# Performance work log

Measured on AMD Instinct MI355X. Metric: run time of the kernel, lower is better.

Reference implementation:

```python
import jax, jax.numpy as jnp
import numpy as np

T, HID, H, KV, D = 2048, 2048, 16, 8, 128
EPS = 1e-6
THETA = 10000.0


def setup_inputs() -> dict:
    key = jax.random.key(0)
    ks = jax.random.split(key, 6)
    positions = jnp.arange(T, dtype=jnp.int64 if jax.config.jax_enable_x64 else jnp.int32)
    hidden_states = jax.random.normal(ks[0], (T, HID), dtype=jnp.float32)
    scale = 0.02
    Wq = jax.random.normal(ks[1], (HID, H * 2 * D), dtype=jnp.float32) * scale
    Wk = jax.random.normal(ks[2], (HID, KV * D), dtype=jnp.float32) * scale
    Wv = jax.random.normal(ks[3], (HID, KV * D), dtype=jnp.float32) * scale
    Wo = jax.random.normal(ks[4], (H * D, HID), dtype=jnp.float32) * scale
    q_norm_w = jnp.zeros((D,), dtype=jnp.float32)  # torch init: zeros, applied as (1+w)
    k_norm_w = jnp.zeros((D,), dtype=jnp.float32)
    return {"positions": positions, "hidden_states": hidden_states, "Wq": Wq,
            "Wk": Wk, "Wv": Wv, "Wo": Wo, "q_norm_w": q_norm_w, "k_norm_w": k_norm_w}


def _rms_norm(x, w):
    # fp32 RMSNorm with (1 + weight) scaling, per last dim
    xf = x.astype(jnp.float32)
    inv = jax.lax.rsqrt(jnp.mean(xf * xf, axis=-1, keepdims=True) + EPS)
    return (xf * inv * (1.0 + w.astype(jnp.float32))).astype(x.dtype)


def _rope(x, positions):
    # neox-style rotary over full head_dim; x: (T, heads, D)
    half = D // 2
    inv_freq = 1.0 / (THETA ** (jnp.arange(0, half, dtype=jnp.float32) / half))
    freqs = positions.astype(jnp.float32)[:, None] * inv_freq  # (T, half)
    cos = jnp.cos(freqs)[:, None, :]  # (T,1,half)
    sin = jnp.sin(freqs)[:, None, :]
    x1, x2 = x[..., :half], x[..., half:]
    return jnp.concatenate([x1 * cos - x2 * sin, x2 * cos + x1 * sin], axis=-1)


def reference(positions, hidden_states, Wq, Wk, Wv, Wo, q_norm_w, k_norm_w):
    scaling = D ** -0.5
    qg = (hidden_states @ Wq).reshape(T, H, 2 * D)
    q, gate = qg[..., :D], qg[..., D:]              # (T,H,D) each
    k = (hidden_states @ Wk).reshape(T, KV, D)
    v = (hidden_states @ Wv).reshape(T, KV, D)
    q = _rms_norm(q, q_norm_w)
    k = _rms_norm(k, k_norm_w)
    q = _rope(q, positions)
    k = _rope(k, positions)
    # GQA: repeat kv heads
    rep = H // KV
    k = jnp.repeat(k, rep, axis=1)                   # (T,H,D)
    v = jnp.repeat(v, rep, axis=1)
    scores = jnp.einsum('thd,shd->hts', q, k) * scaling  # (H,T,T)
    causal = positions[:, None] >= positions[None, :]     # (T,T)
    scores = jnp.where(causal[None], scores, jnp.finfo(scores.dtype).min)
    probs = jax.nn.softmax(scores, axis=-1)
    o = jnp.einsum('hts,shd->thd', probs, v).reshape(T, H * D)
    o = o * jax.nn.sigmoid(gate.reshape(T, H * D))
    return o @ Wo
```

## Files before the change

kernel.cpp:

```cpp
#include <hip/hip_runtime.h>
#include <stdint.h>
#include <math.h>

#define T_SEQ 2048
#define HID   2048
#define NH    16
#define NKV   8
#define DH    128

typedef __bf16 bf16x8 __attribute__((ext_vector_type(8)));
typedef float  f32x4  __attribute__((ext_vector_type(4)));

__device__ __forceinline__ ushort f2bf(float f) {
  uint32_t u = __float_as_uint(f);
  u += 0x7FFF + ((u >> 16) & 1);
  return (ushort)(u >> 16);
}
__device__ __forceinline__ ushort f2bf_rz(float f) {
  return (ushort)(__float_as_uint(f) >> 16);
}
__device__ __forceinline__ float bf2f(ushort u) {
  return __uint_as_float(((uint32_t)u) << 16);
}
__device__ __forceinline__ void gld16(const void* g, void* l) {
  __builtin_amdgcn_global_load_lds(
      (const __attribute__((address_space(1))) uint32_t*)g,
      (__attribute__((address_space(3))) uint32_t*)l, 16, 0, 0);
}

__global__ __launch_bounds__(256) void prep_kernel(
    const float* __restrict__ hs, const float* __restrict__ Wq,
    const float* __restrict__ Wk, const float* __restrict__ Wv,
    const float* __restrict__ Wo, ushort* __restrict__ hs16,
    ushort* __restrict__ Wqt, ushort* __restrict__ Wkt,
    ushort* __restrict__ Wvt, ushort* __restrict__ Wot) {
  int bid = blockIdx.x;
  if (bid < 4096) {
    int i = (bid * 256 + threadIdx.x) * 4;
    float4 v = *(const float4*)(hs + i);
    ushort4 o = {f2bf(v.x), f2bf(v.y), f2bf(v.z), f2bf(v.w)};
    *(ushort4*)(hs16 + i) = o;
    return;
  }
  bid -= 4096;
  const float* src; ushort* dst; int N, bi, bj;
  if (bid < 2048)      { src = Wq; dst = Wqt; N = 4096; bj = bid & 63; bi = bid >> 6; }
  else if (bid < 2560) { bid -= 2048; src = Wk; dst = Wkt; N = 1024; bj = bid & 15; bi = bid >> 4; }
  else if (bid < 3072) { bid -= 2560; src = Wv; dst = Wvt; N = 1024; bj = bid & 15; bi = bid >> 4; }
  else                 { bid -= 3072; src = Wo; dst = Wot; N = 2048; bj = bid & 31; bi = bid >> 5; }
  __shared__ float tile[64][65];
  const int r = threadIdx.x >> 2, cg = (threadIdx.x & 3) * 16;
  const float* sp = src + (size_t)(bi * 64 + r) * N + bj * 64 + cg;
#pragma unroll
  for (int p = 0; p < 4; ++p) {
    float4 v = *(const float4*)(sp + p * 4);
    tile[r][cg + p * 4 + 0] = v.x; tile[r][cg + p * 4 + 1] = v.y;
    tile[r][cg + p * 4 + 2] = v.z; tile[r][cg + p * 4 + 3] = v.w;
  }
  __syncthreads();
  ushort* dp = dst + (size_t)(bj * 64 + r) * HID + bi * 64 + cg;
#pragma unroll
  for (int p = 0; p < 2; ++p) {
    union { uint4 v; ushort u[8]; } o;
#pragma unroll
    for (int j = 0; j < 8; ++j) o.u[j] = f2bf(tile[cg + p * 8 + j][r]);
    *(uint4*)(dp + p * 8) = o.v;
  }
}

template <int MI>
__device__ __forceinline__ void gemm_loop(
    const ushort* __restrict__ A, const ushort* __restrict__ Bt,
    int K, int m0, int n0, ushort* As, ushort* Bs, f32x4 (*acc)[4]) {
  const int tid = threadIdx.x, lane = tid & 63, w = tid >> 6;
  const int quad = lane >> 4, l15 = lane & 15;
  const int wm = (w >> 1) * (MI * 16), wn = (w & 1) * 64;
  const int srow = tid >> 2, sch = tid & 3;
  for (int k0 = 0; k0 < K; k0 += 32) {
    __syncthreads();
#pragma unroll
    for (int p = 0; p < MI / 2; ++p) {
      int row = p * 64 + srow;
      int gch = sch ^ ((row >> 1) & 3);
      gld16(A + (size_t)(m0 + row) * K + k0 + gch * 8,
            As + (p * 256 + w * 64) * 8);
    }
#pragma unroll
    for (int p = 0; p < 2; ++p) {
      int row = p * 64 + srow;
      int gch = sch ^ ((row >> 1) & 3);
      gld16(Bt + (size_t)(n0 + row) * K + k0 + gch * 8,
            Bs + (p * 256 + w * 64) * 8);
    }
    __syncthreads();
    bf16x8 af[MI], bfr[4];
#pragma unroll
    for (int mi = 0; mi < MI; ++mi) {
      int row = wm + mi * 16 + l15;
      int pch = quad ^ ((row >> 1) & 3);
      af[mi] = *(const bf16x8*)(As + row * 32 + pch * 8);
    }
#pragma unroll
    for (int ni = 0; ni < 4; ++ni) {
      int row = wn + ni * 16 + l15;
      int pch = quad ^ ((row >> 1) & 3);
      bfr[ni] = *(const bf16x8*)(Bs + row * 32 + pch * 8);
    }
#pragma unroll
    for (int mi = 0; mi < MI; ++mi)
#pragma unroll
      for (int ni = 0; ni < 4; ++ni)
        acc[mi][ni] = __builtin_amdgcn_mfma_f32_16x16x32_bf16(
            af[mi], bfr[ni], acc[mi][ni], 0, 0, 0);
  }
}

__device__ __forceinline__ void bf16_store(f32x4 (*acc)[4],
                                           ushort* __restrict__ Cb, int Ncols,
                                           int m0, int n0) {
  const int lane = threadIdx.x & 63, w = threadIdx.x >> 6;
  const int quad = lane >> 4, l15 = lane & 15;
  const int wm = (w >> 1) * 64, wn = (w & 1) * 64;
#pragma unroll
  for (int mi = 0; mi < 4; ++mi)
#pragma unroll
    for (int ni = 0; ni < 4; ++ni)
#pragma unroll
      for (int r = 0; r < 4; ++r) {
        int row = m0 + wm + mi * 16 + quad * 4 + r;
        int col = n0 + wn + ni * 16 + l15;
        Cb[(size_t)row * Ncols + col] = f2bf(acc[mi][ni][r]);
      }
}

__global__ __launch_bounds__(256) void gemm_qkv(
    const ushort* __restrict__ hs16, const ushort* __restrict__ Wqt,
    const ushort* __restrict__ Wkt, const ushort* __restrict__ Wvt,
    ushort* __restrict__ q16, ushort* __restrict__ gate16,
    ushort* __restrict__ k16, ushort* __restrict__ v16t) {
  __shared__ ushort As[128 * 32];
  __shared__ ushort Bs[128 * 32];
  f32x4 acc[4][4];
#pragma unroll
  for (int i = 0; i < 4; ++i)
#pragma unroll
    for (int j = 0; j < 4; ++j) acc[i][j] = (f32x4){0.f, 0.f, 0.f, 0.f};
  const int b = blockIdx.x;
  if (b < 512) {
    int mt = b >> 5, nt = b & 31, m0 = mt * 128;
    gemm_loop<4>(hs16, Wqt, HID, m0, nt * 128, As, Bs, acc);
    ushort* dst = ((nt & 1) == 0) ? q16 : gate16;
    bf16_store(acc, dst, NH * DH, m0, (nt >> 1) * 128);
  } else if (b < 640) {
    int f = b - 512, m0 = (f >> 3) * 128, n0 = (f & 7) * 128;
    gemm_loop<4>(hs16, Wkt, HID, m0, n0, As, Bs, acc);
    bf16_store(acc, k16, 1024, m0, n0);
  } else {
    int f = b - 640, m0 = (f >> 4) * 128, n0 = (f & 15) * 128;
    gemm_loop<4>(Wvt, hs16, HID, m0, n0, As, Bs, acc);
    bf16_store(acc, v16t, T_SEQ, m0, n0);
  }
}

__global__ __launch_bounds__(256) void gemm_out(
    const ushort* __restrict__ ob16, const ushort* __restrict__ Wot,
    float* __restrict__ out) {
  __shared__ ushort As[64 * 32];
  __shared__ ushort Bs[128 * 32];
  f32x4 acc[2][4];
#pragma unroll
  for (int i = 0; i < 2; ++i)
#pragma unroll
    for (int j = 0; j < 4; ++j) acc[i][j] = (f32x4){0.f, 0.f, 0.f, 0.f};
  const int b = blockIdx.x;
  const int m0 = (b >> 4) * 64, n0 = (b & 15) * 128;
  gemm_loop<2>(ob16, Wot, HID, m0, n0, As, Bs, acc);
  const int lane = threadIdx.x & 63, w = threadIdx.x >> 6;
  const int quad = lane >> 4, l15 = lane & 15;
  const int wm = (w >> 1) * 32, wn = (w & 1) * 64;
#pragma unroll
  for (int mi = 0; mi < 2; ++mi)
#pragma unroll
    for (int ni = 0; ni < 4; ++ni)
#pragma unroll
      for (int r = 0; r < 4; ++r) {
        int row = m0 + wm + mi * 16 + quad * 4 + r;
        int col = n0 + wn + ni * 16 + l15;
        out[(size_t)row * HID + col] = acc[mi][ni][r];
      }
}

__global__ __launch_bounds__(256) void norm_rope_fast(
    ushort* __restrict__ q16, ushort* __restrict__ k16,
    const int* __restrict__ positions, const float* __restrict__ qw,
    const float* __restrict__ kw) {
  const int tid = threadIdx.x, lg = tid & 15;
  const int r = blockIdx.x * 16 + (tid >> 4);
  ushort* x; const float* wgt; int t;
  if (r < T_SEQ * NH) { t = r >> 4; x = q16 + (size_t)r * DH; wgt = qw; }
  else { int rr = r - T_SEQ * NH; t = rr >> 3; x = k16 + (size_t)rr * DH; wgt = kw; }

  ushort* xp = x + lg * 8;
  ushort4 a = *(const ushort4*)(xp);
  ushort4 bq = *(const ushort4*)(xp + 4);
  float xv[8] = {bf2f(a.x), bf2f(a.y), bf2f(a.z), bf2f(a.w),
                 bf2f(bq.x), bf2f(bq.y), bf2f(bq.z), bf2f(bq.w)};

  float ss = 0.f;
#pragma unroll
  for (int j = 0; j < 8; ++j) ss += xv[j] * xv[j];
  ss += __shfl_xor(ss, 1, 16);
  ss += __shfl_xor(ss, 2, 16);
  ss += __shfl_xor(ss, 4, 16);
  ss += __shfl_xor(ss, 8, 16);
  const float rstd = rsqrtf(ss * (1.f / 128.f) + 1e-6f);

  const int dbase = lg * 8;
  float xn[8];
#pragma unroll
  for (int j = 0; j < 8; ++j) xn[j] = xv[j] * rstd * (1.f + wgt[dbase + j]);

  float pr[8];
#pragma unroll
  for (int j = 0; j < 8; ++j) pr[j] = __shfl_xor(xn[j], 8, 16);

  const float pos = (float)positions[t];
  const int dh = dbase & 63;
  const bool lo = (lg < 8);
  ushort o[8];
#pragma unroll
  for (int j = 0; j < 8; ++j) {
    float rev = pos * exp2f((float)(dh + j) * -0.20762050593045233f) *
                0.15915494309189535f;
    float fr = rev - floorf(rev);
    float s = __builtin_amdgcn_sinf(fr);
    float c = __builtin_amdgcn_cosf(fr);
    float out = lo ? (xn[j] * c - pr[j] * s) : (xn[j] * c + pr[j] * s);
    o[j] = f2bf(out);
  }
  *(ushort4*)(xp)     = (ushort4){o[0], o[1], o[2], o[3]};
  *(ushort4*)(xp + 4) = (ushort4){o[4], o[5], o[6], o[7]};
}

__global__ __launch_bounds__(256) void attn_mfma(
    const ushort* __restrict__ q16, const ushort* __restrict__ k16,
    const ushort* __restrict__ v16t, const float* __restrict__ qnw,
    const float* __restrict__ knw, ushort* __restrict__ Op0,
    ushort* __restrict__ Op1, ushort* __restrict__ Op2,
    float* __restrict__ lpart) {
  const int pb = blockIdx.x, h = blockIdx.y, s = blockIdx.z, kvh = h >> 1;
  const int tid = threadIdx.x, lane = tid & 63, w = tid >> 6;
  const int quad = lane >> 4, l15 = lane & 15;

  __shared__ ushort Ks[64 * 128];
  __shared__ ushort Vs[144 * 64];
  __shared__ ushort Ps[4][16][72];

  for (int i = tid; i < 16 * 64; i += 256) {
    int row = 128 + (i >> 6), col = i & 63;
    Vs[row * 64 + col] = (row == 128) ? (ushort)0x3F80 : (ushort)0;
  }

  __shared__ float s8[8];
  __shared__ float bshare;
  {
    float mq = 0.f, mk = 0.f;
    if (tid < 128) { mq = fabsf(1.f + qnw[tid]); mk = fabsf(1.f + knw[tid]); }
#pragma unroll
    for (int off = 32; off >= 1; off >>= 1) {
      mq = fmaxf(mq, __shfl_xor(mq, off, 64));
      mk = fmaxf(mk, __shfl_xor(mk, off, 64));
    }
    if (lane == 0) { s8[w * 2] = mq; s8[w * 2 + 1] = mk; }
    __syncthreads();
    if (tid == 0) {
      float MQ = fmaxf(s8[0], s8[2]), MK = fmaxf(s8[1], s8[3]);
      bshare = 16.3217f * MQ * MK * 1.02f + 0.1f;
    }
    __syncthreads();
  }
  const float B = bshare;
  const float CSC = 0.08838834764831845f * 1.44269504088896f;

#pragma unroll 1
  for (int sel = 0; sel < 2; ++sel) {
    const int qt = sel ? (31 - pb) : pb;
    const int q0 = qt * 64;
    const int ntl = (qt >= s) ? ((qt - s) / 3 + 1) : 0;

    bf16x8 qf[4];
    const ushort* qbase = q16 + ((size_t)(q0 + w * 16 + l15) * NH + h) * DH;
#pragma unroll
    for (int ks = 0; ks < 4; ++ks)
      qf[ks] = *(const bf16x8*)(qbase + ks * 32 + quad * 8);

    f32x4 oacc[9];
#pragma unroll
    for (int i = 0; i < 9; ++i) oacc[i] = (f32x4){0.f, 0.f, 0.f, 0.f};

#pragma unroll 1
    for (int it = 0; it < ntl; ++it) {
      const int kt = s + 3 * it;
      const int kt0 = kt * 64;
      __syncthreads();
#pragma unroll
      for (int p = 0; p < 4; ++p) {
        int row = p * 16 + (tid >> 4), ch = tid & 15;
        int gch = ch ^ (row & 15);
        gld16(k16 + ((size_t)(kt0 + row) * NKV + kvh) * DH + gch * 8,
              Ks + (p * 256 + w * 64) * 8);
      }
#pragma unroll
      for (int p = 0; p < 4; ++p) {
        int row = p * 32 + (tid >> 3), ch = tid & 7;
        int gch = ch ^ (row & 7);
        gld16(v16t + (size_t)(kvh * DH + row) * T_SEQ + kt0 + gch * 8,
              Vs + (p * 256 + w * 64) * 8);
      }
      __syncthreads();

      f32x4 sacc[4];
#pragma unroll
      for (int ni = 0; ni < 4; ++ni) sacc[ni] = (f32x4){0.f, 0.f, 0.f, 0.f};
#pragma unroll
      for (int ks = 0; ks < 4; ++ks)
#pragma unroll
        for (int ni = 0; ni < 4; ++ni) {
          int row = ni * 16 + l15;
          int pch = (ks * 4 + quad) ^ (row & 15);
          bf16x8 kf = *(const bf16x8*)(Ks + row * 128 + pch * 8);
          sacc[ni] = __builtin_amdgcn_mfma_f32_16x16x32_bf16(
              qf[ks], kf, sacc[ni], 0, 0, 0);
        }

      const bool diag = (kt == qt);
#pragma unroll
      for (int ni = 0; ni < 4; ++ni) {
        int key = kt0 + ni * 16 + l15;
#pragma unroll
        for (int r = 0; r < 4; ++r) {
          float arg = fmaf(sacc[ni][r], CSC, -B);
          float pv;
          if (diag) {
            int q = q0 + w * 16 + quad * 4 + r;
            pv = (key <= q) ? exp2f(arg) : 0.f;
          } else {
            pv = exp2f(arg);
          }
          Ps[w][quad * 4 + r][ni * 16 + l15] = f2bf_rz(pv);
        }
      }

#pragma unroll
      for (int ks2 = 0; ks2 < 2; ++ks2) {
        bf16x8 pf = *(const bf16x8*)(&Ps[w][l15][ks2 * 32 + quad * 8]);
#pragma unroll
        for (int ni = 0; ni < 9; ++ni) {
          int row = ni * 16 + l15;
          int pch = (ks2 * 4 + quad) ^ (row & 7);
          bf16x8 vf = *(const bf16x8*)(Vs + row * 64 + pch * 8);
          oacc[ni] = __builtin_amdgcn_mfma_f32_16x16x32_bf16(
              pf, vf, oacc[ni], 0, 0, 0);
        }
      }
    }

    ushort* Op = (s == 0) ? Op0 : (s == 1) ? Op1 : Op2;
#pragma unroll
    for (int ni = 0; ni < 8; ++ni) {
      int d = ni * 16 + l15;
#pragma unroll
      for (int r = 0; r < 4; ++r) {
        int q = q0 + w * 16 + quad * 4 + r;
        Op[((size_t)h * T_SEQ + q) * DH + d] = f2bf(oacc[ni][r]);
      }
    }
    if (l15 == 0) {
#pragma unroll
      for (int r = 0; r < 4; ++r) {
        int q = q0 + w * 16 + quad * 4 + r;
        lpart[(size_t)s * (NH * T_SEQ) + h * T_SEQ + q] = oacc[8][r];
      }
    }
  }
}

__global__ __launch_bounds__(256) void combine_kernel(
    const ushort* __restrict__ Op0, const ushort* __restrict__ Op1,
    const ushort* __restrict__ Op2, const float* __restrict__ lpart,
    const ushort* __restrict__ gate16, ushort* __restrict__ ob16) {
  const int t = blockIdx.x, tid = threadIdx.x;
  const int h = tid >> 4, d0 = (tid & 15) * 8;
  const int NT = NH * T_SEQ;
  const float l = lpart[h * T_SEQ + t] + lpart[NT + h * T_SEQ + t] +
                  lpart[2 * NT + h * T_SEQ + t];
  const float inv = 1.0f / l;
  const size_t po = ((size_t)h * T_SEQ + t) * DH + d0;
  ushort4 a0 = *(const ushort4*)(Op0 + po);
  ushort4 a1 = *(const ushort4*)(Op0 + po + 4);
  ushort4 b0 = *(const ushort4*)(Op1 + po);
  ushort4 b1 = *(const ushort4*)(Op1 + po + 4);
  ushort4 c0 = *(const ushort4*)(Op2 + po);
  ushort4 c1 = *(const ushort4*)(Op2 + po + 4);
  const ushort* gp = gate16 + (size_t)t * (NH * DH) + h * DH + d0;
  ushort4 g0 = *(const ushort4*)(gp);
  ushort4 g1 = *(const ushort4*)(gp + 4);
  float oa[8] = {bf2f(a0.x), bf2f(a0.y), bf2f(a0.z), bf2f(a0.w),
                 bf2f(a1.x), bf2f(a1.y), bf2f(a1.z), bf2f(a1.w)};
  float ob[8] = {bf2f(b0.x), bf2f(b0.y), bf2f(b0.z), bf2f(b0.w),
                 bf2f(b1.x), bf2f(b1.y), bf2f(b1.z), bf2f(b1.w)};
  float oc[8] = {bf2f(c0.x), bf2f(c0.y), bf2f(c0.z), bf2f(c0.w),
                 bf2f(c1.x), bf2f(c1.y), bf2f(c1.z), bf2f(c1.w)};
  float gg[8] = {bf2f(g0.x), bf2f(g0.y), bf2f(g0.z), bf2f(g0.w),
                 bf2f(g1.x), bf2f(g1.y), bf2f(g1.z), bf2f(g1.w)};
  ushort r[8];
#pragma unroll
  for (int i = 0; i < 8; ++i) {
    float o = (oa[i] + ob[i] + oc[i]) * inv;
    o = o / (1.0f + exp2f(-gg[i] * 1.44269504088896f));
    r[i] = f2bf(o);
  }
  ushort* op = ob16 + (size_t)t * (NH * DH) + h * DH + d0;
  *(ushort4*)(op)     = (ushort4){r[0], r[1], r[2], r[3]};
  *(ushort4*)(op + 4) = (ushort4){r[4], r[5], r[6], r[7]};
}

extern "C" void kernel_launch(void* const* d_in, const int* in_sizes, int n_in,
                              void* d_out, int out_size, void* d_ws, size_t ws_size,
                              hipStream_t stream) {
  const int*   positions = (const int*)d_in[0];
  const float* hs  = (const float*)d_in[1];
  const float* Wq  = (const float*)d_in[2];
  const float* Wk  = (const float*)d_in[3];
  const float* Wv  = (const float*)d_in[4];
  const float* Wo  = (const float*)d_in[5];
  const float* qnw = (const float*)d_in[6];
  const float* knw = (const float*)d_in[7];
  float* out = (float*)d_out;

  const size_t MB = 1 << 20;
  uint8_t* ws = (uint8_t*)d_ws;
  ushort* hs16  = (ushort*)(ws + 0);
  ushort* Op0   = (ushort*)(ws + 0);
  ushort* Wqt   = (ushort*)(ws + 8 * MB);
  ushort* Op1   = (ushort*)(ws + 8 * MB);
  ushort* Op2   = (ushort*)(ws + 16 * MB);
  ushort* Wkt   = (ushort*)(ws + 24 * MB);
  ushort* ob16  = (ushort*)(ws + 24 * MB);
  ushort* Wvt   = (ushort*)(ws + 28 * MB);
  ushort* v16t  = (ushort*)(ws + 32 * MB);
  ushort* k16   = (ushort*)(ws + 36 * MB);
  ushort* q16   = (ushort*)(ws + 40 * MB);
  ushort* gate16= (ushort*)(ws + 48 * MB);
  ushort* Wot   = (ushort*)(ws + 56 * MB);
  float*  lpart = (float*)d_out;

  prep_kernel<<<8192, 256, 0, stream>>>(hs, Wq, Wk, Wv, Wo,
                                        hs16, Wqt, Wkt, Wvt, Wot);
  gemm_qkv<<<768, 256, 0, stream>>>(hs16, Wqt, Wkt, Wvt,
                                    q16, gate16, k16, v16t);
  norm_rope_fast<<<3072, 256, 0, stream>>>(q16, k16, positions, qnw, knw);
  attn_mfma<<<dim3(16, NH, 3), 256, 0, stream>>>(q16, k16, v16t, qnw, knw,
                                                 Op0, Op1, Op2, lpart);
  combine_kernel<<<T_SEQ, 256, 0, stream>>>(Op0, Op1, Op2, lpart, gate16, ob16);
  gemm_out<<<512, 256, 0, stream>>>(ob16, Wot, out);
}
```

Measured before the change: 269.4 us.

## Double-buffer K/V tiles in attention and reduce key split from three to two

The attention kernel now prefetches the next K/V tile into a second shared-memory buffer while computing on the current one, using manual vmcnt waits and barriers in place of two syncthreads per iteration. The key-dimension split drops from 3 to 2 partitions, so the grid shrinks to 512 blocks and the combine kernel reads one fewer partial output. The ones-row used for the row-sum moves into a separate LDS array. The cost is double the K/V LDS footprint, which may lower occupancy, and fewer blocks with more work each.

```diff
diff --git a/kernel.cpp b/kernel.cpp
--- a/kernel.cpp
+++ b/kernel.cpp
@@ -242,24 +242,43 @@
   *(ushort4*)(xp + 4) = (ushort4){o[4], o[5], o[6], o[7]};
 }
 
+__device__ __forceinline__ void stage_kv(const ushort* __restrict__ k16,
+                                         const ushort* __restrict__ v16t,
+                                         int kvh, int kt0, ushort* Ksb,
+                                         ushort* Vsb, int tid) {
+  const int w = tid >> 6;
+#pragma unroll
+  for (int p = 0; p < 4; ++p) {
+    int row = p * 16 + (tid >> 4), ch = tid & 15;
+    int gch = ch ^ (row & 15);
+    gld16(k16 + ((size_t)(kt0 + row) * NKV + kvh) * DH + gch * 8,
+          Ksb + (p * 256 + w * 64) * 8);
+  }
+#pragma unroll
+  for (int p = 0; p < 4; ++p) {
+    int row = p * 32 + (tid >> 3), ch = tid & 7;
+    int gch = ch ^ (row & 7);
+    gld16(v16t + (size_t)(kvh * DH + row) * T_SEQ + kt0 + gch * 8,
+          Vsb + (p * 256 + w * 64) * 8);
+  }
+}
+
 __global__ __launch_bounds__(256) void attn_mfma(
     const ushort* __restrict__ q16, const ushort* __restrict__ k16,
     const ushort* __restrict__ v16t, const float* __restrict__ qnw,
     const float* __restrict__ knw, ushort* __restrict__ Op0,
-    ushort* __restrict__ Op1, ushort* __restrict__ Op2,
-    float* __restrict__ lpart) {
+    ushort* __restrict__ Op1, float* __restrict__ lpart) {
   const int pb = blockIdx.x, h = blockIdx.y, s = blockIdx.z, kvh = h >> 1;
   const int tid = threadIdx.x, lane = tid & 63, w = tid >> 6;
   const int quad = lane >> 4, l15 = lane & 15;
 
-  __shared__ ushort Ks[64 * 128];
-  __shared__ ushort Vs[144 * 64];
+  __shared__ ushort Ks[2][64 * 128];
+  __shared__ ushort Vs[2][128 * 64];
+  __shared__ ushort Ones[16 * 64];
   __shared__ ushort Ps[4][16][72];
 
-  for (int i = tid; i < 16 * 64; i += 256) {
-    int row = 128 + (i >> 6), col = i & 63;
-    Vs[row * 64 + col] = (row == 128) ? (ushort)0x3F80 : (ushort)0;
-  }
+  for (int i = tid; i < 16 * 64; i += 256)
+    Ones[i] = (i < 64) ? (ushort)0x3F80 : (ushort)0;
 
   __shared__ float s8[8];
   __shared__ float bshare;
@@ -286,7 +305,7 @@
   for (int sel = 0; sel < 2; ++sel) {
     const int qt = sel ? (31 - pb) : pb;
     const int q0 = qt * 64;
-    const int ntl = (qt >= s) ? ((qt - s) / 3 + 1) : 0;
+    const int ntl = (qt >= s) ? ((qt - s) / 2 + 1) : 0;
 
     bf16x8 qf[4];
     const ushort* qbase = q16 + ((size_t)(q0 + w * 16 + l15) * NH + h) * DH;
@@ -298,26 +317,20 @@
 #pragma unroll
     for (int i = 0; i < 9; ++i) oacc[i] = (f32x4){0.f, 0.f, 0.f, 0.f};
 
+    if (ntl > 0) stage_kv(k16, v16t, kvh, s * 64, Ks[0], Vs[0], tid);
+
 #pragma unroll 1
     for (int it = 0; it < ntl; ++it) {
-      const int kt = s + 3 * it;
+      const int kt = s + 2 * it;
       const int kt0 = kt * 64;
-      __syncthreads();
-#pragma unroll
-      for (int p = 0; p < 4; ++p) {
-        int row = p * 16 + (tid >> 4), ch = tid & 15;
-        int gch = ch ^ (row & 15);
-        gld16(k16 + ((size_t)(kt0 + row) * NKV + kvh) * DH + gch * 8,
-              Ks + (p * 256 + w * 64) * 8);
-      }
-#pragma unroll
-      for (int p = 0; p < 4; ++p) {
-        int row = p * 32 + (tid >> 3), ch = tid & 7;
-        int gch = ch ^ (row & 7);
-        gld16(v16t + (size_t)(kvh * DH + row) * T_SEQ + kt0 + gch * 8,
-              Vs + (p * 256 + w * 64) * 8);
-      }
-      __syncthreads();
+      const int cur = it & 1;
+      if (it + 1 < ntl) {
+        stage_kv(k16, v16t, kvh, (kt + 2) * 64, Ks[cur ^ 1], Vs[cur ^ 1], tid);
+        asm volatile("s_waitcnt vmcnt(8)" ::: "memory");
+      } else {
+        asm volatile("s_waitcnt vmcnt(0)" ::: "memory");
+      }
+      asm volatile("s_barrier" ::: "memory");
 
       f32x4 sacc[4];
 #pragma unroll
@@ -328,7 +341,7 @@
         for (int ni = 0; ni < 4; ++ni) {
           int row = ni * 16 + l15;
           int pch = (ks * 4 + quad) ^ (row & 15);
-          bf16x8 kf = *(const bf16x8*)(Ks + row * 128 + pch * 8);
+          bf16x8 kf = *(const bf16x8*)(&Ks[cur][row * 128 + pch * 8]);
           sacc[ni] = __builtin_amdgcn_mfma_f32_16x16x32_bf16(
               qf[ks], kf, sacc[ni], 0, 0, 0);
         }
@@ -358,14 +371,17 @@
         for (int ni = 0; ni < 9; ++ni) {
           int row = ni * 16 + l15;
           int pch = (ks2 * 4 + quad) ^ (row & 7);
-          bf16x8 vf = *(const bf16x8*)(Vs + row * 64 + pch * 8);
+          const ushort* vp = (ni < 8) ? &Vs[cur][row * 64 + pch * 8]
+                                      : &Ones[l15 * 64 + pch * 8];
+          bf16x8 vf = *(const bf16x8*)(vp);
           oacc[ni] = __builtin_amdgcn_mfma_f32_16x16x32_bf16(
               pf, vf, oacc[ni], 0, 0, 0);
         }
       }
-    }
-
-    ushort* Op = (s == 0) ? Op0 : (s == 1) ? Op1 : Op2;
+      asm volatile("s_barrier" ::: "memory");
+    }
+
+    ushort* Op = s ? Op1 : Op0;
 #pragma unroll
     for (int ni = 0; ni < 8; ++ni) {
       int d = ni * 16 + l15;
@@ -387,21 +403,18 @@
 
 __global__ __launch_bounds__(256) void combine_kernel(
     const ushort* __restrict__ Op0, const ushort* __restrict__ Op1,
-    const ushort* __restrict__ Op2, const float* __restrict__ lpart,
-    const ushort* __restrict__ gate16, ushort* __restrict__ ob16) {
+    const float* __restrict__ lpart, const ushort* __restrict__ gate16,
+    ushort* __restrict__ ob16) {
   const int t = blockIdx.x, tid = threadIdx.x;
   const int h = tid >> 4, d0 = (tid & 15) * 8;
   const int NT = NH * T_SEQ;
-  const float l = lpart[h * T_SEQ + t] + lpart[NT + h * T_SEQ + t] +
-                  lpart[2 * NT + h * T_SEQ + t];
+  const float l = lpart[h * T_SEQ + t] + lpart[NT + h * T_SEQ + t];
   const float inv = 1.0f / l;
   const size_t po = ((size_t)h * T_SEQ + t) * DH + d0;
   ushort4 a0 = *(const ushort4*)(Op0 + po);
   ushort4 a1 = *(const ushort4*)(Op0 + po + 4);
   ushort4 b0 = *(const ushort4*)(Op1 + po);
   ushort4 b1 = *(const ushort4*)(Op1 + po + 4);
-  ushort4 c0 = *(const ushort4*)(Op2 + po);
-  ushort4 c1 = *(const ushort4*)(Op2 + po + 4);
   const ushort* gp = gate16 + (size_t)t * (NH * DH) + h * DH + d0;
   ushort4 g0 = *(const ushort4*)(gp);
   ushort4 g1 = *(const ushort4*)(gp + 4);
@@ -409,14 +422,12 @@
                  bf2f(a1.x), bf2f(a1.y), bf2f(a1.z), bf2f(a1.w)};
   float ob[8] = {bf2f(b0.x), bf2f(b0.y), bf2f(b0.z), bf2f(b0.w),
                  bf2f(b1.x), bf2f(b1.y), bf2f(b1.z), bf2f(b1.w)};
-  float oc[8] = {bf2f(c0.x), bf2f(c0.y), bf2f(c0.z), bf2f(c0.w),
-                 bf2f(c1.x), bf2f(c1.y), bf2f(c1.z), bf2f(c1.w)};
   float gg[8] = {bf2f(g0.x), bf2f(g0.y), bf2f(g0.z), bf2f(g0.w),
                  bf2f(g1.x), bf2f(g1.y), bf2f(g1.z), bf2f(g1.w)};
   ushort r[8];
 #pragma unroll
   for (int i = 0; i < 8; ++i) {
-    float o = (oa[i] + ob[i] + oc[i]) * inv;
+    float o = (oa[i] + ob[i]) * inv;
     o = o / (1.0f + exp2f(-gg[i] * 1.44269504088896f));
     r[i] = f2bf(o);
   }
@@ -444,7 +455,6 @@
   ushort* Op0   = (ushort*)(ws + 0);
   ushort* Wqt   = (ushort*)(ws + 8 * MB);
   ushort* Op1   = (ushort*)(ws + 8 * MB);
-  ushort* Op2   = (ushort*)(ws + 16 * MB);
   ushort* Wkt   = (ushort*)(ws + 24 * MB);
   ushort* ob16  = (ushort*)(ws + 24 * MB);
   ushort* Wvt   = (ushort*)(ws + 28 * MB);
@@ -460,8 +470,8 @@
   gemm_qkv<<<768, 256, 0, stream>>>(hs16, Wqt, Wkt, Wvt,
                                     q16, gate16, k16, v16t);
   norm_rope_fast<<<3072, 256, 0, stream>>>(q16, k16, positions, qnw, knw);
-  attn_mfma<<<dim3(16, NH, 3), 256, 0, stream>>>(q16, k16, v16t, qnw, knw,
-                                                 Op0, Op1, Op2, lpart);
-  combine_kernel<<<T_SEQ, 256, 0, stream>>>(Op0, Op1, Op2, lpart, gate16, ob16);
+  attn_mfma<<<dim3(16, NH, 2), 256, 0, stream>>>(q16, k16, v16t, qnw, knw,
+                                                 Op0, Op1, lpart);
+  combine_kernel<<<T_SEQ, 256, 0, stream>>>(Op0, Op1, lpart, gate16, ob16);
   gemm_out<<<512, 256, 0, stream>>>(ob16, Wot, out);
 }
```

Result: no change. 272.4 us (+1.1%).
